# Optimization experiments

Hardware: AMD Instinct MI355X
Metric: run time of the kernel (lower is better)

## Reference

```python
import jax, jax.numpy as jnp
import numpy as np

N = 50000          # nodes
E = 800000         # directed edges
F_IN = 64          # input feature dim
H = 64             # GCN hidden dim
DH = 32            # decoder hidden dim


def setup_inputs() -> dict:
    key = jax.random.key(0)
    ks = jax.random.split(key, 10)
    x = jax.random.normal(ks[0], (N, F_IN), dtype=jnp.float32)
    edge_index = jax.random.randint(ks[1], (2, E), 0, N, dtype=jnp.int64)
    s = 0.1  # weight init scale
    return {
        "x": x,
        "edge_index": edge_index,
        "W1": jax.random.normal(ks[2], (F_IN, H), dtype=jnp.float32) * s,
        "b1": jnp.zeros((H,), dtype=jnp.float32),
        "W2": jax.random.normal(ks[3], (H, H), dtype=jnp.float32) * s,
        "b2": jnp.zeros((H,), dtype=jnp.float32),
        "Wd1": jax.random.normal(ks[4], (H, DH), dtype=jnp.float32) * s,
        "bd1": jnp.zeros((DH,), dtype=jnp.float32),
        "Wd2": jax.random.normal(ks[5], (DH, 1), dtype=jnp.float32) * s,
        "bd2": jnp.zeros((1,), dtype=jnp.float32),
    }


def _gcn_conv(x, src, dst, norm, W, b, n):
    # transform then gather-scale-scatter (PyG GCNConv message passing)
    h = x @ W                                   # (n, out)
    msg = h[src] * norm[:, None]                # (E+n, out) gather on src
    out = jax.ops.segment_sum(msg, dst, num_segments=n)  # scatter-add on dst
    return out + b


def reference(x, edge_index, W1, b1, W2, b2, Wd1, bd1, Wd2, bd2):
    n = x.shape[0]
    # add self-loops (GCNConv default)
    loops = jnp.arange(n, dtype=edge_index.dtype)
    src = jnp.concatenate([edge_index[0], loops])
    dst = jnp.concatenate([edge_index[1], loops])
    # symmetric normalization D^{-1/2} A D^{-1/2}, degree on dst incl. self-loops
    deg = jax.ops.segment_sum(jnp.ones_like(dst, dtype=x.dtype), dst, num_segments=n)
    dinv = jnp.where(deg > 0, deg ** -0.5, 0.0)
    norm = dinv[src] * dinv[dst]                # (E+n,)
    h = jax.nn.relu(_gcn_conv(x, src, dst, norm, W1, b1, n))
    # gcn_dropout is identity in eval mode
    h = jax.nn.relu(_gcn_conv(h, src, dst, norm, W2, b2, n))
    h = jax.nn.relu(h @ Wd1 + bd1)              # decoder MLP
    pred = (h @ Wd2 + bd2).squeeze(-1)          # (N,)
    return pred
```

## Files before the change

### kernel.cpp

```cpp
#include <hip/hip_runtime.h>

#define NF 64

__device__ __forceinline__ float rlf(float v, int l) {
    return __int_as_float(__builtin_amdgcn_readlane(__float_as_int(v), l));
}


__global__ void count_deg(const int* __restrict__ dst, int* __restrict__ cnt, int E) {
    int e = blockIdx.x * blockDim.x + threadIdx.x;
    if (e < E) atomicAdd(&cnt[dst[e]], 1);
}

__global__ __launch_bounds__(1024) void scan_rowptr(const int* __restrict__ cnt,
                                                    int* __restrict__ rowptr, int n) {
    __shared__ int wsum[16];
    __shared__ int wexcl[16];
    __shared__ int carry_s;
    int tid = threadIdx.x, lane = tid & 63, w = tid >> 6;
    if (tid == 0) carry_s = 0;
    __syncthreads();
    for (int base = 0; base < n; base += 1024) {
        int i = base + tid;
        int v = (i < n) ? cnt[i] : 0;
        int inc = v;
#pragma unroll
        for (int d = 1; d < 64; d <<= 1) {
            int t = __shfl_up(inc, d);
            if (lane >= d) inc += t;
        }
        if (lane == 63) wsum[w] = inc;
        __syncthreads();
        if (w == 0 && lane < 16) {
            int s = wsum[lane];
            int e2 = s;
#pragma unroll
            for (int d = 1; d < 16; d <<= 1) {
                int t = __shfl_up(e2, d);
                if (lane >= d) e2 += t;
            }
            wexcl[lane] = e2 - s;
        }
        __syncthreads();
        int carry = carry_s;
        int excl = carry + wexcl[w] + inc - v;
        if (i < n) rowptr[i] = excl;
        if (i == n - 1) rowptr[n] = excl + v;
        __syncthreads();
        if (tid == 1023) carry_s = carry + wexcl[15] + wsum[15];
        __syncthreads();
    }
}

__global__ void dinv_fill(const int* __restrict__ cnt, float* __restrict__ dinv,
                          int* __restrict__ fill, int n) {
    int i = blockIdx.x * blockDim.x + threadIdx.x;
    if (i < n) {
        dinv[i] = rsqrtf((float)(cnt[i] + 1));
        fill[i] = 0;
    }
}

__global__ void fill_csr(const int* __restrict__ src, const int* __restrict__ dst,
                         const int* __restrict__ rowptr, int* __restrict__ fill,
                         const float* __restrict__ dinv, int2* __restrict__ pairs, int E) {
    int e = blockIdx.x * blockDim.x + threadIdx.x;
    if (e >= E) return;
    int d = dst[e], s = src[e];
    int pos = rowptr[d] + atomicAdd(&fill[d], 1);
    pairs[pos] = make_int2(s, __float_as_int(dinv[s]));
}


template <bool DEC>
__global__ __launch_bounds__(256) void gcn_layer(
    const int2* __restrict__ pairs, const int* __restrict__ rowptr,
    const float* __restrict__ dinv, const float* __restrict__ xin,
    const float* __restrict__ W, const float* __restrict__ bias,
    float* __restrict__ xout,
    const float* __restrict__ Wd1, const float* __restrict__ bd1,
    const float* __restrict__ Wd2, const float* __restrict__ bd2,
    float* __restrict__ pred, int n)
{
    __shared__ float Wd1l[64][32];
    __shared__ float bd1l[32];
    __shared__ float w2l[32];
    int tid = threadIdx.x;
    int lane = tid & 63;
    if (DEC) {
        for (int i = tid; i < 2048; i += 256) Wd1l[i >> 5][i & 31] = Wd1[i];
        if (tid < 32) { bd1l[tid] = bd1[tid]; w2l[tid] = Wd2[tid]; }
    }
    __syncthreads();

    float wcol[64];
#pragma unroll
    for (int k = 0; k < 64; ++k) wcol[k] = W[k * NF + lane];
    float bv = bias[lane];
    float bd2v = DEC ? bd2[0] : 0.0f;

    int wid = blockIdx.x * 4 + (tid >> 6);
    int nw = gridDim.x * 4;
    for (int i = wid; i < n; i += nw) {
        float di = dinv[i];
        float a = xin[(size_t)i * NF + lane] * di * di;

        int jb = __builtin_amdgcn_readfirstlane(rowptr[i]);
        int je = __builtin_amdgcn_readfirstlane(rowptr[i + 1]);
        for (int base = jb; base < je; base += 64) {
            int cnt = min(64, je - base);
            int2 p = make_int2(0, 0);
            if (base + lane < je) p = pairs[base + lane];
            int e = 0;
            for (; e + 3 < cnt; e += 4) {
                int s0 = __builtin_amdgcn_readlane(p.x, e);
                int s1 = __builtin_amdgcn_readlane(p.x, e + 1);
                int s2 = __builtin_amdgcn_readlane(p.x, e + 2);
                int s3 = __builtin_amdgcn_readlane(p.x, e + 3);
                float w0 = __int_as_float(__builtin_amdgcn_readlane(p.y, e)) * di;
                float w1 = __int_as_float(__builtin_amdgcn_readlane(p.y, e + 1)) * di;
                float w2 = __int_as_float(__builtin_amdgcn_readlane(p.y, e + 2)) * di;
                float w3 = __int_as_float(__builtin_amdgcn_readlane(p.y, e + 3)) * di;
                float v0 = xin[(size_t)s0 * NF + lane];
                float v1 = xin[(size_t)s1 * NF + lane];
                float v2 = xin[(size_t)s2 * NF + lane];
                float v3 = xin[(size_t)s3 * NF + lane];
                a = fmaf(v0, w0, a);
                a = fmaf(v1, w1, a);
                a = fmaf(v2, w2, a);
                a = fmaf(v3, w3, a);
            }
            for (; e < cnt; ++e) {
                int s0 = __builtin_amdgcn_readlane(p.x, e);
                float w0 = __int_as_float(__builtin_amdgcn_readlane(p.y, e)) * di;
                a = fmaf(xin[(size_t)s0 * NF + lane], w0, a);
            }
        }

        float o = bv;
#pragma unroll
        for (int k = 0; k < 64; ++k) o = fmaf(rlf(a, k), wcol[k], o);
        o = fmaxf(o, 0.0f);

        if (!DEC) {
            xout[(size_t)i * NF + lane] = o;
        } else {
            int j = lane & 31;
            float s = 0.0f;
#pragma unroll
            for (int k = 0; k < 64; ++k) s = fmaf(rlf(o, k), Wd1l[k][j], s);
            float hj = fmaxf(s + bd1l[j], 0.0f);
            float pp = hj * w2l[j];
#pragma unroll
            for (int m = 16; m >= 1; m >>= 1) pp += __shfl_xor(pp, m);
            if (lane == 0) pred[i] = pp + bd2v;
        }
    }
}


extern "C" void kernel_launch(void* const* d_in, const int* in_sizes, int n_in,
                              void* d_out, int out_size, void* d_ws, size_t ws_size,
                              hipStream_t stream) {
    const float* x   = (const float*)d_in[0];
    const int*   ei  = (const int*)d_in[1];
    const float* W1  = (const float*)d_in[2];
    const float* b1  = (const float*)d_in[3];
    const float* W2  = (const float*)d_in[4];
    const float* b2  = (const float*)d_in[5];
    const float* Wd1 = (const float*)d_in[6];
    const float* bd1 = (const float*)d_in[7];
    const float* Wd2 = (const float*)d_in[8];
    const float* bd2 = (const float*)d_in[9];
    float* pred = (float*)d_out;

    const int N = in_sizes[0] / NF;
    const int E = in_sizes[1] / 2;
    const int* src = ei;
    const int* dst = ei + E;

    char* ws = (char*)d_ws;
    size_t off = 0;
    int*   cnt    = (int*)(ws + off);   off += (size_t)4 * N;
    int*   rowptr = (int*)(ws + off);   off += (size_t)4 * (N + 1);
    int*   fill   = (int*)(ws + off);   off += (size_t)4 * N;
    float* dinv   = (float*)(ws + off); off += (size_t)4 * N;
    off = (off + 7) & ~(size_t)7;
    int2*  pairs  = (int2*)(ws + off);  off += (size_t)8 * E;
    float* h1     = (float*)(ws + off);

    const int B = 256;
    const int eb = (E + B - 1) / B;
    const int nb = (N + B - 1) / B;

    hipMemsetAsync(cnt, 0, (size_t)4 * N, stream);
    count_deg<<<eb, B, 0, stream>>>(dst, cnt, E);
    scan_rowptr<<<1, 1024, 0, stream>>>(cnt, rowptr, N);
    dinv_fill<<<nb, B, 0, stream>>>(cnt, dinv, fill, N);
    fill_csr<<<eb, B, 0, stream>>>(src, dst, rowptr, fill, dinv, pairs, E);

    const int gb = 1536;

    gcn_layer<false><<<gb, B, 0, stream>>>(pairs, rowptr, dinv, x, W1, b1, h1,
                                           Wd1, bd1, Wd2, bd2, pred, N);
    gcn_layer<true><<<gb, B, 0, stream>>>(pairs, rowptr, dinv, h1, W2, b2, h1,
                                          Wd1, bd1, Wd2, bd2, pred, N);
}
```

Measured before the change: 346.4 us.

## Parallelize rowptr scan across blocks and gather four edges per wave with float4

Replaces the single-block serial scan over all nodes with a three-kernel block scan (per-block scan, scan of block sums, add-back fused with dinv/fill init). In the GCN layer, each wave now splits into four 16-lane quarters that each gather a different neighbor row as float4, then reduces the quarters with cross-lane shuffles before the matvec. This aims to cut the latency of the one-block scan and raise memory-level parallelism and load width in the gather, at the cost of an extra kernel launch and shuffle reductions.

```diff
diff --git a/kernel.cpp b/kernel.cpp
--- a/kernel.cpp
+++ b/kernel.cpp
@@ -12,51 +12,74 @@
     if (e < E) atomicAdd(&cnt[dst[e]], 1);
 }
 
-__global__ __launch_bounds__(1024) void scan_rowptr(const int* __restrict__ cnt,
-                                                    int* __restrict__ rowptr, int n) {
+__global__ __launch_bounds__(1024) void scan_blk(const int* __restrict__ cnt,
+                                                 int* __restrict__ rowptr,
+                                                 int* __restrict__ bsum, int n) {
     __shared__ int wsum[16];
     __shared__ int wexcl[16];
-    __shared__ int carry_s;
     int tid = threadIdx.x, lane = tid & 63, w = tid >> 6;
-    if (tid == 0) carry_s = 0;
-    __syncthreads();
-    for (int base = 0; base < n; base += 1024) {
-        int i = base + tid;
-        int v = (i < n) ? cnt[i] : 0;
-        int inc = v;
-#pragma unroll
-        for (int d = 1; d < 64; d <<= 1) {
-            int t = __shfl_up(inc, d);
-            if (lane >= d) inc += t;
-        }
-        if (lane == 63) wsum[w] = inc;
-        __syncthreads();
-        if (w == 0 && lane < 16) {
-            int s = wsum[lane];
-            int e2 = s;
-#pragma unroll
-            for (int d = 1; d < 16; d <<= 1) {
-                int t = __shfl_up(e2, d);
-                if (lane >= d) e2 += t;
-            }
-            wexcl[lane] = e2 - s;
-        }
-        __syncthreads();
-        int carry = carry_s;
-        int excl = carry + wexcl[w] + inc - v;
-        if (i < n) rowptr[i] = excl;
-        if (i == n - 1) rowptr[n] = excl + v;
-        __syncthreads();
-        if (tid == 1023) carry_s = carry + wexcl[15] + wsum[15];
-        __syncthreads();
-    }
-}
-
-__global__ void dinv_fill(const int* __restrict__ cnt, float* __restrict__ dinv,
-                          int* __restrict__ fill, int n) {
+    int i = blockIdx.x * 1024 + tid;
+    int v = (i < n) ? cnt[i] : 0;
+    int inc = v;
+#pragma unroll
+    for (int d = 1; d < 64; d <<= 1) {
+        int t = __shfl_up(inc, d);
+        if (lane >= d) inc += t;
+    }
+    if (lane == 63) wsum[w] = inc;
+    __syncthreads();
+    if (w == 0 && lane < 16) {
+        int s = wsum[lane];
+        int e2 = s;
+#pragma unroll
+        for (int d = 1; d < 16; d <<= 1) {
+            int t = __shfl_up(e2, d);
+            if (lane >= d) e2 += t;
+        }
+        wexcl[lane] = e2 - s;
+    }
+    __syncthreads();
+    if (i < n) rowptr[i] = wexcl[w] + inc - v;
+    if (tid == 1023) bsum[blockIdx.x] = wexcl[15] + wsum[15];
+}
+
+__global__ __launch_bounds__(1024) void scan_part(int* __restrict__ bsum, int nb) {
+    __shared__ int wsum[16];
+    __shared__ int wexcl[16];
+    int tid = threadIdx.x, lane = tid & 63, w = tid >> 6;
+    int v = (tid < nb) ? bsum[tid] : 0;
+    int inc = v;
+#pragma unroll
+    for (int d = 1; d < 64; d <<= 1) {
+        int t = __shfl_up(inc, d);
+        if (lane >= d) inc += t;
+    }
+    if (lane == 63) wsum[w] = inc;
+    __syncthreads();
+    if (w == 0 && lane < 16) {
+        int s = wsum[lane];
+        int e2 = s;
+#pragma unroll
+        for (int d = 1; d < 16; d <<= 1) {
+            int t = __shfl_up(e2, d);
+            if (lane >= d) e2 += t;
+        }
+        wexcl[lane] = e2 - s;
+    }
+    __syncthreads();
+    if (tid < nb) bsum[tid] = wexcl[w] + inc - v;
+}
+
+__global__ void scan_add(int* __restrict__ rowptr, const int* __restrict__ bsum,
+                         const int* __restrict__ cnt, float* __restrict__ dinv,
+                         int* __restrict__ fill, int n) {
     int i = blockIdx.x * blockDim.x + threadIdx.x;
     if (i < n) {
-        dinv[i] = rsqrtf((float)(cnt[i] + 1));
+        int c = cnt[i];
+        int r = rowptr[i] + bsum[i >> 10];
+        rowptr[i] = r;
+        if (i == n - 1) rowptr[n] = r + c;
+        dinv[i] = rsqrtf((float)(c + 1));
         fill[i] = 0;
     }
 }
@@ -99,47 +122,46 @@
     float bv = bias[lane];
     float bd2v = DEC ? bd2[0] : 0.0f;
 
+    int q = lane >> 4;
+    int fl = (lane & 15) * 4;
+
     int wid = blockIdx.x * 4 + (tid >> 6);
     int nw = gridDim.x * 4;
     for (int i = wid; i < n; i += nw) {
         float di = dinv[i];
-        float a = xin[(size_t)i * NF + lane] * di * di;
-
         int jb = __builtin_amdgcn_readfirstlane(rowptr[i]);
         int je = __builtin_amdgcn_readfirstlane(rowptr[i + 1]);
+
+        float4 sv = *reinterpret_cast<const float4*>(xin + (size_t)i * NF + fl);
+        float wself = (q == 0) ? di * di : 0.0f;
+        float a[4];
+        a[0] = sv.x * wself; a[1] = sv.y * wself;
+        a[2] = sv.z * wself; a[3] = sv.w * wself;
+
         for (int base = jb; base < je; base += 64) {
             int cnt = min(64, je - base);
             int2 p = make_int2(0, 0);
             if (base + lane < je) p = pairs[base + lane];
-            int e = 0;
-            for (; e + 3 < cnt; e += 4) {
-                int s0 = __builtin_amdgcn_readlane(p.x, e);
-                int s1 = __builtin_amdgcn_readlane(p.x, e + 1);
-                int s2 = __builtin_amdgcn_readlane(p.x, e + 2);
-                int s3 = __builtin_amdgcn_readlane(p.x, e + 3);
-                float w0 = __int_as_float(__builtin_amdgcn_readlane(p.y, e)) * di;
-                float w1 = __int_as_float(__builtin_amdgcn_readlane(p.y, e + 1)) * di;
-                float w2 = __int_as_float(__builtin_amdgcn_readlane(p.y, e + 2)) * di;
-                float w3 = __int_as_float(__builtin_amdgcn_readlane(p.y, e + 3)) * di;
-                float v0 = xin[(size_t)s0 * NF + lane];
-                float v1 = xin[(size_t)s1 * NF + lane];
-                float v2 = xin[(size_t)s2 * NF + lane];
-                float v3 = xin[(size_t)s3 * NF + lane];
-                a = fmaf(v0, w0, a);
-                a = fmaf(v1, w1, a);
-                a = fmaf(v2, w2, a);
-                a = fmaf(v3, w3, a);
+            for (int e = 0; e < cnt; e += 4) {
+                int sl = e + q;
+                int s = __shfl(p.x, sl);
+                float wgt = __int_as_float(__shfl(p.y, sl)) * di;
+                float4 v = *reinterpret_cast<const float4*>(xin + (size_t)s * NF + fl);
+                a[0] = fmaf(v.x, wgt, a[0]);
+                a[1] = fmaf(v.y, wgt, a[1]);
+                a[2] = fmaf(v.z, wgt, a[2]);
+                a[3] = fmaf(v.w, wgt, a[3]);
             }
-            for (; e < cnt; ++e) {
-                int s0 = __builtin_amdgcn_readlane(p.x, e);
-                float w0 = __int_as_float(__builtin_amdgcn_readlane(p.y, e)) * di;
-                a = fmaf(xin[(size_t)s0 * NF + lane], w0, a);
-            }
+        }
+#pragma unroll
+        for (int j = 0; j < 4; ++j) {
+            a[j] += __shfl_xor(a[j], 16);
+            a[j] += __shfl_xor(a[j], 32);
         }
 
         float o = bv;
 #pragma unroll
-        for (int k = 0; k < 64; ++k) o = fmaf(rlf(a, k), wcol[k], o);
+        for (int k = 0; k < 64; ++k) o = fmaf(rlf(a[k & 3], k >> 2), wcol[k], o);
         o = fmaxf(o, 0.0f);
 
         if (!DEC) {
@@ -185,18 +207,21 @@
     int*   rowptr = (int*)(ws + off);   off += (size_t)4 * (N + 1);
     int*   fill   = (int*)(ws + off);   off += (size_t)4 * N;
     float* dinv   = (float*)(ws + off); off += (size_t)4 * N;
-    off = (off + 7) & ~(size_t)7;
+    int*   bsum   = (int*)(ws + off);   off += (size_t)4 * 1024;
+    off = (off + 15) & ~(size_t)15;
     int2*  pairs  = (int2*)(ws + off);  off += (size_t)8 * E;
     float* h1     = (float*)(ws + off);
 
     const int B = 256;
     const int eb = (E + B - 1) / B;
     const int nb = (N + B - 1) / B;
+    const int nb1024 = (N + 1023) / 1024;
 
     hipMemsetAsync(cnt, 0, (size_t)4 * N, stream);
     count_deg<<<eb, B, 0, stream>>>(dst, cnt, E);
-    scan_rowptr<<<1, 1024, 0, stream>>>(cnt, rowptr, N);
-    dinv_fill<<<nb, B, 0, stream>>>(cnt, dinv, fill, N);
+    scan_blk<<<nb1024, 1024, 0, stream>>>(cnt, rowptr, bsum, N);
+    scan_part<<<1, 1024, 0, stream>>>(bsum, nb1024);
+    scan_add<<<nb, B, 0, stream>>>(rowptr, bsum, cnt, dinv, fill, N);
     fill_csr<<<eb, B, 0, stream>>>(src, dst, rowptr, fill, dinv, pairs, E);
 
     const int gb = 1536;
```

Result: faster. 280.4 us (-19.1%).
